# Kernel optimization log

Measured on AMD Instinct MI355X. Metric: run time of the kernel, lower is better.

Reference implementation:

```python
import jax, jax.numpy as jnp
import numpy as np

B, S, DIM = 64, 256, 512
H = 16
DH = DIM // H          # 32
W = 256                # window_size == seq_len
ROPE_BASE = 10000.0


def _rope(x):
    # x: (B, S, H, DH), interleaved-pair RoPE
    pos = jnp.arange(S, dtype=jnp.float32)
    inv_freq = 1.0 / (ROPE_BASE ** (jnp.arange(0, DH, 2, dtype=jnp.float32) / DH))
    sinusoid = pos[:, None] * inv_freq[None, :]            # (S, DH/2)
    sin = jnp.sin(sinusoid)[None, :, None, :]              # (1, S, 1, DH/2)
    cos = jnp.cos(sinusoid)[None, :, None, :]
    x1 = x[..., 0::2]
    x2 = x[..., 1::2]
    r1 = x1 * cos - x2 * sin
    r2 = x1 * sin + x2 * cos
    return jnp.stack([r1, r2], axis=-1).reshape(x.shape)


def setup_inputs() -> dict:
    key = jax.random.key(0)
    ks = jax.random.split(key, 8)
    s = 1.0 / np.sqrt(DIM)
    return {
        "hidden_states": jax.random.normal(ks[0], (B, S, DIM), jnp.float32),
        "Wq": jax.random.normal(ks[1], (DIM, DIM), jnp.float32) * s,
        "bq": jnp.zeros((DIM,), jnp.float32),
        "Wk": jax.random.normal(ks[2], (DIM, DIM), jnp.float32) * s,
        "bk": jnp.zeros((DIM,), jnp.float32),
        "Wv": jax.random.normal(ks[3], (DIM, DIM), jnp.float32) * s,
        "bv": jnp.zeros((DIM,), jnp.float32),
        "bias_table": jax.random.normal(ks[4], (2 * W - 1, H), jnp.float32) * 0.02,
    }


def reference(hidden_states, Wq, bq, Wk, bk, Wv, bv, bias_table):
    b, s, _ = hidden_states.shape
    q = hidden_states @ Wq + bq
    k = hidden_states @ Wk + bk
    v = hidden_states @ Wv + bv
    # (B, S, H, DH)
    q = _rope(q.reshape(b, s, H, DH))
    k = _rope(k.reshape(b, s, H, DH))
    v = v.reshape(b, s, H, DH)
    # (B, H, S, DH)
    q = q.transpose(0, 2, 1, 3)
    k = k.transpose(0, 2, 1, 3)
    v = v.transpose(0, 2, 1, 3)
    scores = jnp.einsum('bhqd,bhkd->bhqk', q, k) / np.sqrt(DH)
    # relative_position_index[i, j] == (i - j) + W - 1
    rel_idx = jnp.arange(W)[:, None] - jnp.arange(W)[None, :] + (W - 1)
    rel_bias = bias_table[rel_idx]                 # (W, W, H)
    rel_bias = rel_bias.transpose(2, 0, 1)[None]   # (1, H, W, W)
    # NOTE: bias added AFTER softmax, faithful to the original module
    probs = jax.nn.softmax(scores, axis=-1) + rel_bias
    ctx = jnp.einsum('bhqk,bhkd->bhqd', probs, v)
    ctx = ctx.transpose(0, 2, 1, 3).reshape(b, s, DIM)
    return ctx
```

## Files before the change

### kernel.cpp

```cpp
#include <hip/hip_runtime.h>
#include <stdint.h>

typedef __attribute__((ext_vector_type(8))) short bf16x8;
typedef __attribute__((ext_vector_type(4))) float f32x4;
typedef __attribute__((ext_vector_type(4))) unsigned int u32x4;

#define MFMA16(a, b, c) __builtin_amdgcn_mfma_f32_16x16x32_bf16(a, b, c, 0, 0, 0)

__device__ __forceinline__ float bf2f(unsigned short u) {
    union { unsigned int i; float f; } x; x.i = ((unsigned int)u) << 16; return x.f;
}
__device__ __forceinline__ unsigned short f2bf(float f) {
    union { float f; unsigned int i; } x; x.f = f;
    unsigned int u = x.i;
    return (unsigned short)((u + 0x7FFFu + ((u >> 16) & 1u)) >> 16);
}

__global__ __launch_bounds__(256) void k_cvt(const float4* __restrict__ in,
                                             unsigned short* __restrict__ out) {
    int i = blockIdx.x * 256 + threadIdx.x;
    float4 v = in[i];
    ushort4 o;
    o.x = f2bf(v.x); o.y = f2bf(v.y); o.z = f2bf(v.z); o.w = f2bf(v.w);
    *(ushort4*)(out + (size_t)i * 4) = o;
}

__global__ __launch_bounds__(256) void k_wt(const float* __restrict__ W0,
                                            const float* __restrict__ W1,
                                            const float* __restrict__ W2,
                                            unsigned short* __restrict__ Wt2) {
    int tile = blockIdx.x * 4 + (threadIdx.x >> 6);
    int l = threadIdx.x & 63;
    int nt = tile >> 4;
    int kb = tile & 15;
    int mat = nt >> 5;
    const float* __restrict__ Wm = (mat == 0) ? W0 : (mat == 1) ? W1 : W2;
    int np = (nt & 31) * 16 + (l & 15);
    int k0 = kb * 32 + (l >> 4) * 8;
    bf16x8 o;
#pragma unroll
    for (int e = 0; e < 8; ++e) o[e] = (short)f2bf(Wm[(size_t)(k0 + e) * 512 + np]);
    *(bf16x8*)(Wt2 + (size_t)tile * 512 + l * 8) = o;
}

__global__ __launch_bounds__(256) void k_sc(float* __restrict__ cs2) {
    int s = threadIdx.x;
    for (int f = 0; f < 16; ++f) {
        float inv = powf(10000.0f, -(float)f / 16.0f);
        float a = (float)s * inv;
        cs2[(s * 16 + f) * 2 + 0] = cosf(a);
        cs2[(s * 16 + f) * 2 + 1] = sinf(a);
    }
}

__global__ __launch_bounds__(256, 2) void k_gemm(
    const unsigned short* __restrict__ A,
    const unsigned short* __restrict__ Bt,
    const float* __restrict__ bq, const float* __restrict__ bk, const float* __restrict__ bv,
    const float* __restrict__ cs2,
    unsigned short* __restrict__ Qo, unsigned short* __restrict__ Ko, unsigned short* __restrict__ Vo) {
    __shared__ unsigned short a_l[2][8192];
    const int tid = threadIdx.x;
    const int wave = tid >> 6, lane = tid & 63;
    const int l15 = lane & 15, l4 = lane >> 4;
    int bid = blockIdx.x;
    int swz = (bid & 7) * 192 + (bid >> 3);
    const int m0 = (swz / 12) * 128;
    const int n0 = (swz % 12) * 128;
    const int wm = (wave >> 1) * 64, wn = (wave & 1) * 64;
    const bool isV = (n0 >= 1024);

    f32x4 zero4 = {0.f, 0.f, 0.f, 0.f};
    f32x4 acc[4][4];
#pragma unroll
    for (int i = 0; i < 4; ++i)
#pragma unroll
        for (int j = 0; j < 4; ++j) acc[i][j] = zero4;

    const int srow = tid >> 3;
    const int skc = ((tid & 7) ^ (srow & 7)) * 8;
    const unsigned short* ga = A + (size_t)(m0 + srow) * 512 + skc;
    const unsigned short* gB2 = Bt + ((size_t)((n0 + wn) >> 4) << 13) + lane * 8;

#define STAGE(buf, kt)                                                                          \
    {                                                                                           \
        const unsigned short* pa = ga + (kt) * 64;                                              \
        unsigned short* la = &a_l[(buf)][wave * 512];                                           \
        _Pragma("unroll")                                                                       \
        for (int it = 0; it < 4; ++it) {                                                        \
            __builtin_amdgcn_global_load_lds(                                                   \
                (const __attribute__((address_space(1))) unsigned int*)(pa + it * (32 * 512)),  \
                (__attribute__((address_space(3))) unsigned int*)(la + it * 2048), 16, 0, 0);   \
        }                                                                                       \
    }
#define LOADB(breg, kt)                                                                         \
    {                                                                                           \
        _Pragma("unroll")                                                                       \
        for (int kc = 0; kc < 2; ++kc)                                                          \
            _Pragma("unroll")                                                                   \
            for (int j = 0; j < 4; ++j)                                                         \
                breg[kc][j] = *(const bf16x8*)(gB2 + j * 8192 + (kt) * 1024 + kc * 512);        \
    }
#define COMPUTE(buf, breg)                                                                      \
    {                                                                                           \
        _Pragma("unroll")                                                                       \
        for (int kc = 0; kc < 2; ++kc) {                                                        \
            bf16x8 af[4];                                                                       \
            int g = ((kc * 4 + l4) ^ (l15 & 7)) * 8;                                            \
            _Pragma("unroll")                                                                   \
            for (int i = 0; i < 4; ++i)                                                         \
                af[i] = *(const bf16x8*)&a_l[(buf)][(wm + i * 16 + l15) * 64 + g];              \
            if (!isV) {                                                                         \
                _Pragma("unroll")                                                               \
                for (int i = 0; i < 4; ++i)                                                     \
                    _Pragma("unroll")                                                           \
                    for (int j = 0; j < 4; ++j)                                                 \
                        acc[i][j] = MFMA16(af[i], breg[kc][j], acc[i][j]);                      \
            } else {                                                                            \
                _Pragma("unroll")                                                               \
                for (int i = 0; i < 4; ++i)                                                     \
                    _Pragma("unroll")                                                           \
                    for (int j = 0; j < 4; ++j)                                                 \
                        acc[i][j] = MFMA16(breg[kc][j], af[i], acc[i][j]);                      \
            }                                                                                   \
        }                                                                                       \
    }
#define SYNC() { asm volatile("s_waitcnt vmcnt(0) lgkmcnt(0)" ::: "memory");                    \
                 __builtin_amdgcn_s_barrier(); }

    bf16x8 b0[2][4], b1[2][4];
    LOADB(b0, 0);
    STAGE(0, 0);
    for (int kt2 = 0; kt2 < 8; kt2 += 2) {
        SYNC();
        LOADB(b1, kt2 + 1);
        STAGE(1, kt2 + 1);
        COMPUTE(0, b0);
        SYNC();
        if (kt2 + 2 < 8) {
            LOADB(b0, kt2 + 2);
            STAGE(0, kt2 + 2);
        }
        COMPUTE(1, b1);
    }
#undef STAGE
#undef LOADB
#undef COMPUTE
#undef SYNC

    if (!isV) {
        const int mat = n0 >> 9;
        unsigned short* __restrict__ dst = (mat == 0) ? Qo : Ko;
        const float* __restrict__ bias = (mat == 0) ? bq : bk;
#pragma unroll
        for (int j = 0; j < 4; ++j) {
            int col = (n0 & 511) + wn + j * 16 + l15;
            float bb = bias[col];
            int h = col >> 5, dh = col & 31, f = dh >> 1;
            float sgn = (col & 1) ? 1.0f : -1.0f;
#pragma unroll
            for (int i = 0; i < 4; ++i) {
#pragma unroll
                for (int r = 0; r < 4; ++r) {
                    int m = m0 + wm + i * 16 + l4 * 4 + r;
                    int b2 = m >> 8, s = m & 255;
                    float t = acc[i][j][r] + bb;
                    float partner = __shfl_xor(t, 1);
                    float2 cn = *(const float2*)(cs2 + (s * 16 + f) * 2);
                    float o = t * cn.x + sgn * partner * cn.y;
                    dst[(size_t)(b2 * 16 + h) * 8192 + s * 32 + dh] = f2bf(o);
                }
            }
        }
    } else {
#pragma unroll
        for (int j = 0; j < 4; ++j) {
#pragma unroll
            for (int r = 0; r < 4; ++r) {
                int n = (n0 & 511) + wn + j * 16 + l4 * 4 + r;
                float bb = bv[n];
                int h = n >> 5, dh = n & 31;
#pragma unroll
                for (int i = 0; i < 4; ++i) {
                    int m = m0 + wm + i * 16 + l15;
                    int b2 = m >> 8, s = m & 255;
                    Vo[(size_t)(b2 * 16 + h) * 8192 + dh * 256 + s] = f2bf(acc[i][j][r] + bb);
                }
            }
        }
    }
}

__global__ __launch_bounds__(256, 2) void k_attn(
    const unsigned short* __restrict__ Qm, const unsigned short* __restrict__ Km,
    const unsigned short* __restrict__ Vm,
    const float* __restrict__ bias_table, float* __restrict__ out) {
    __shared__ unsigned short k_l[256 * 32];
    __shared__ unsigned short vt_l[32 * 256];
    __shared__ unsigned short p_l[64 * 264];
    __shared__ float bias_g[512];

    const int tid = threadIdx.x, wave = tid >> 6, lane = tid & 63;
    const int l15 = lane & 15, l4 = lane >> 4;
    int bid = blockIdx.x;
    int swz = (bid & 7) * 128 + (bid >> 3);
    const int h = swz & 15, b = swz >> 4;
    const size_t bh = ((size_t)(b * 16 + h)) * 8192;

    for (int i = tid; i < 511; i += 256) bias_g[i] = bias_table[i * 16 + h];

#pragma unroll
    for (int it = 0; it < 4; ++it) {
        int p = it * 256 + wave * 64 + lane;
        __builtin_amdgcn_global_load_lds(
            (const __attribute__((address_space(1))) unsigned int*)(Km + bh + p * 8),
            (__attribute__((address_space(3))) unsigned int*)(k_l + it * 2048 + wave * 512), 16, 0, 0);
    }
#pragma unroll
    for (int it = 0; it < 4; ++it) {
        int p = it * 256 + wave * 64 + lane;
        int dh = p >> 5, cpos = p & 31;
        int srcc = cpos ^ (dh & 7);
        __builtin_amdgcn_global_load_lds(
            (const __attribute__((address_space(1))) unsigned int*)(Vm + bh + dh * 256 + srcc * 8),
            (__attribute__((address_space(3))) unsigned int*)(vt_l + it * 2048 + wave * 512), 16, 0, 0);
    }
    __syncthreads();

    f32x4 zero4 = {0.f, 0.f, 0.f, 0.f};
    const float SCL2 = 0.17677669529663687f * 1.4426950408889634f;
    const int qrow = 16 * wave + l15;

    for (int qb = 0; qb < 4; ++qb) {
        const int q0 = qb * 64;
        bf16x8 qfrag = *(const bf16x8*)(Qm + bh + (size_t)(q0 + qrow) * 32 + l4 * 8);

        f32x4 sc[16];
#pragma unroll
        for (int ct = 0; ct < 16; ++ct) {
            bf16x8 kf = *(const bf16x8*)&k_l[(ct * 16 + l15) * 32 + l4 * 8];
            sc[ct] = MFMA16(kf, qfrag, zero4);
        }

        float sum = 0.f;
#pragma unroll
        for (int ct = 0; ct < 16; ++ct) {
#pragma unroll
            for (int r = 0; r < 4; ++r) {
                float e;
                float x = sc[ct][r] * SCL2;
                asm("v_exp_f32 %0, %1" : "=v"(e) : "v"(x));
                sc[ct][r] = e;
                sum += e;
            }
        }
        sum += __shfl_xor(sum, 16);
        sum += __shfl_xor(sum, 32);
        float inv = 1.0f / sum;

#pragma unroll
        for (int ct = 0; ct < 16; ++ct) {
            int kbase = 16 * ct + 4 * l4;
            int jb = q0 + qrow - kbase + 255;
            float p0 = sc[ct][0] * inv + bias_g[jb];
            float p1 = sc[ct][1] * inv + bias_g[jb - 1];
            float p2 = sc[ct][2] * inv + bias_g[jb - 2];
            float p3 = sc[ct][3] * inv + bias_g[jb - 3];
            uint2 w;
            w.x = (unsigned int)f2bf(p0) | ((unsigned int)f2bf(p1) << 16);
            w.y = (unsigned int)f2bf(p2) | ((unsigned int)f2bf(p3) << 16);
            *(uint2*)&p_l[qrow * 264 + kbase] = w;
        }

        f32x4 o0 = zero4, o1 = zero4;
#pragma unroll
        for (int kc = 0; kc < 8; ++kc) {
            bf16x8 pf = *(const bf16x8*)&p_l[qrow * 264 + kc * 32 + l4 * 8];
            int vc = (kc * 4 + l4) ^ (l15 & 7);
            bf16x8 v0 = *(const bf16x8*)&vt_l[l15 * 256 + vc * 8];
            bf16x8 v1 = *(const bf16x8*)&vt_l[(16 + l15) * 256 + vc * 8];
            o0 = MFMA16(pf, v0, o0);
            o1 = MFMA16(pf, v1, o1);
        }

#pragma unroll
        for (int r = 0; r < 4; ++r) {
            int s = q0 + 16 * wave + l4 * 4 + r;
            float* po = out + ((size_t)(b * 256 + s)) * 512 + h * 32;
            po[l15] = o0[r];
            po[16 + l15] = o1[r];
        }
    }
}

extern "C" void kernel_launch(void* const* d_in, const int* in_sizes, int n_in,
                              void* d_out, int out_size, void* d_ws, size_t ws_size,
                              hipStream_t stream) {
    const float* hs = (const float*)d_in[0];
    const float* Wq = (const float*)d_in[1];
    const float* bq = (const float*)d_in[2];
    const float* Wk = (const float*)d_in[3];
    const float* bk = (const float*)d_in[4];
    const float* Wv = (const float*)d_in[5];
    const float* bv = (const float*)d_in[6];
    const float* bt = (const float*)d_in[7];
    float* out = (float*)d_out;

    char* ws = (char*)d_ws;
    unsigned short* hsb = (unsigned short*)ws;
    unsigned short* wt = (unsigned short*)(ws + 16777216);
    unsigned short* Qo = (unsigned short*)(ws + 18350080);
    unsigned short* Ko = (unsigned short*)(ws + 35127296);
    unsigned short* Vo = (unsigned short*)(ws + 51904512);
    float* cs2 = (float*)(ws + 68681728);

    hipLaunchKernelGGL(k_cvt, dim3(8192), dim3(256), 0, stream, (const float4*)hs, hsb);
    hipLaunchKernelGGL(k_wt, dim3(384), dim3(256), 0, stream, Wq, Wk, Wv, wt);
    hipLaunchKernelGGL(k_sc, dim3(1), dim3(256), 0, stream, cs2);
    hipLaunchKernelGGL(k_gemm, dim3(1536), dim3(256), 0, stream,
                       hsb, wt, bq, bk, bv, cs2, Qo, Ko, Vo);
    hipLaunchKernelGGL(k_attn, dim3(1024), dim3(256), 0, stream,
                       Qo, Ko, Vo, bt, out);
}
```

Measured before the change: 100.6 us.

## Pre-tile activations for LDS-free GEMM and keep attention probs in registers

The conversion kernel now writes hidden states in an MFMA-fragment-tiled bf16 layout, so the QKV GEMM loads A and B fragments straight from global memory with no LDS staging or barriers. The GEMM tile is halved to 128x64, doubling the grid, and occupancy is raised to 3 blocks per CU. The attention kernel drops the P shared-memory buffer and rearranges the probability fragments across lanes with packed bf16 conversions and xor shuffles, allowing 4 blocks per CU. The risks are more global/L2 traffic from loads that no longer go through LDS, and extra shuffle work in the attention loop.

Measured after the change: 128.6 us. 1.28x slower.

```diff
diff --git a/kernel.cpp b/kernel.cpp
--- a/kernel.cpp
+++ b/kernel.cpp
@@ -17,12 +17,30 @@
 }
 
 __global__ __launch_bounds__(256) void k_cvt(const float4* __restrict__ in,
-                                             unsigned short* __restrict__ out) {
-    int i = blockIdx.x * 256 + threadIdx.x;
-    float4 v = in[i];
-    ushort4 o;
-    o.x = f2bf(v.x); o.y = f2bf(v.y); o.z = f2bf(v.z); o.w = f2bf(v.w);
-    *(ushort4*)(out + (size_t)i * 4) = o;
+                                             unsigned short* __restrict__ At) {
+    __shared__ unsigned short t[16 * 512];
+    const int tid = threadIdx.x;
+    const int blk = blockIdx.x;
+#pragma unroll
+    for (int it = 0; it < 8; ++it) {
+        int idx = it * 256 + tid;
+        int row = idx >> 7, col4 = idx & 127;
+        float4 v = in[(size_t)(blk * 16 + row) * 128 + col4];
+        ushort4 o;
+        o.x = f2bf(v.x); o.y = f2bf(v.y); o.z = f2bf(v.z); o.w = f2bf(v.w);
+        int addr = row * 512 + (((col4 >> 1) ^ (row & 7)) << 3) + ((col4 & 1) << 2);
+        *(ushort4*)&t[addr] = o;
+    }
+    __syncthreads();
+#pragma unroll
+    for (int it = 0; it < 4; ++it) {
+        int idx = it * 256 + tid;
+        int kb = idx >> 6, l = idx & 63;
+        int row = l & 15, l4 = l >> 4;
+        int c = (kb * 4 + l4) ^ (row & 7);
+        bf16x8 v = *(const bf16x8*)&t[row * 512 + c * 8];
+        *(bf16x8*)(At + ((size_t)(blk * 16 + kb) << 9) + l * 8) = v;
+    }
 }
 
 __global__ __launch_bounds__(256) void k_wt(const float* __restrict__ W0,
@@ -53,107 +71,58 @@
     }
 }
 
-__global__ __launch_bounds__(256, 2) void k_gemm(
-    const unsigned short* __restrict__ A,
+__global__ __launch_bounds__(256, 3) void k_gemm(
+    const unsigned short* __restrict__ At,
     const unsigned short* __restrict__ Bt,
     const float* __restrict__ bq, const float* __restrict__ bk, const float* __restrict__ bv,
     const float* __restrict__ cs2,
     unsigned short* __restrict__ Qo, unsigned short* __restrict__ Ko, unsigned short* __restrict__ Vo) {
-    __shared__ unsigned short a_l[2][8192];
     const int tid = threadIdx.x;
     const int wave = tid >> 6, lane = tid & 63;
     const int l15 = lane & 15, l4 = lane >> 4;
     int bid = blockIdx.x;
-    int swz = (bid & 7) * 192 + (bid >> 3);
-    const int m0 = (swz / 12) * 128;
-    const int n0 = (swz % 12) * 128;
-    const int wm = (wave >> 1) * 64, wn = (wave & 1) * 64;
+    int swz = (bid & 7) * 384 + (bid >> 3);
+    const int m0 = (swz / 24) * 128;
+    const int n0 = (swz % 24) * 64;
+    const int wm = (wave >> 1) * 64, wn = (wave & 1) * 32;
     const bool isV = (n0 >= 1024);
 
     f32x4 zero4 = {0.f, 0.f, 0.f, 0.f};
-    f32x4 acc[4][4];
+    f32x4 acc[4][2];
 #pragma unroll
     for (int i = 0; i < 4; ++i)
 #pragma unroll
-        for (int j = 0; j < 4; ++j) acc[i][j] = zero4;
-
-    const int srow = tid >> 3;
-    const int skc = ((tid & 7) ^ (srow & 7)) * 8;
-    const unsigned short* ga = A + (size_t)(m0 + srow) * 512 + skc;
-    const unsigned short* gB2 = Bt + ((size_t)((n0 + wn) >> 4) << 13) + lane * 8;
-
-#define STAGE(buf, kt)                                                                          \
-    {                                                                                           \
-        const unsigned short* pa = ga + (kt) * 64;                                              \
-        unsigned short* la = &a_l[(buf)][wave * 512];                                           \
-        _Pragma("unroll")                                                                       \
-        for (int it = 0; it < 4; ++it) {                                                        \
-            __builtin_amdgcn_global_load_lds(                                                   \
-                (const __attribute__((address_space(1))) unsigned int*)(pa + it * (32 * 512)),  \
-                (__attribute__((address_space(3))) unsigned int*)(la + it * 2048), 16, 0, 0);   \
-        }                                                                                       \
-    }
-#define LOADB(breg, kt)                                                                         \
-    {                                                                                           \
-        _Pragma("unroll")                                                                       \
-        for (int kc = 0; kc < 2; ++kc)                                                          \
-            _Pragma("unroll")                                                                   \
-            for (int j = 0; j < 4; ++j)                                                         \
-                breg[kc][j] = *(const bf16x8*)(gB2 + j * 8192 + (kt) * 1024 + kc * 512);        \
-    }
-#define COMPUTE(buf, breg)                                                                      \
-    {                                                                                           \
-        _Pragma("unroll")                                                                       \
-        for (int kc = 0; kc < 2; ++kc) {                                                        \
-            bf16x8 af[4];                                                                       \
-            int g = ((kc * 4 + l4) ^ (l15 & 7)) * 8;                                            \
-            _Pragma("unroll")                                                                   \
-            for (int i = 0; i < 4; ++i)                                                         \
-                af[i] = *(const bf16x8*)&a_l[(buf)][(wm + i * 16 + l15) * 64 + g];              \
-            if (!isV) {                                                                         \
-                _Pragma("unroll")                                                               \
-                for (int i = 0; i < 4; ++i)                                                     \
-                    _Pragma("unroll")                                                           \
-                    for (int j = 0; j < 4; ++j)                                                 \
-                        acc[i][j] = MFMA16(af[i], breg[kc][j], acc[i][j]);                      \
-            } else {                                                                            \
-                _Pragma("unroll")                                                               \
-                for (int i = 0; i < 4; ++i)                                                     \
-                    _Pragma("unroll")                                                           \
-                    for (int j = 0; j < 4; ++j)                                                 \
-                        acc[i][j] = MFMA16(breg[kc][j], af[i], acc[i][j]);                      \
-            }                                                                                   \
-        }                                                                                       \
-    }
-#define SYNC() { asm volatile("s_waitcnt vmcnt(0) lgkmcnt(0)" ::: "memory");                    \
-                 __builtin_amdgcn_s_barrier(); }
-
-    bf16x8 b0[2][4], b1[2][4];
-    LOADB(b0, 0);
-    STAGE(0, 0);
-    for (int kt2 = 0; kt2 < 8; kt2 += 2) {
-        SYNC();
-        LOADB(b1, kt2 + 1);
-        STAGE(1, kt2 + 1);
-        COMPUTE(0, b0);
-        SYNC();
-        if (kt2 + 2 < 8) {
-            LOADB(b0, kt2 + 2);
-            STAGE(0, kt2 + 2);
-        }
-        COMPUTE(1, b1);
-    }
-#undef STAGE
-#undef LOADB
-#undef COMPUTE
-#undef SYNC
+        for (int j = 0; j < 2; ++j) acc[i][j] = zero4;
+
+    const unsigned short* gA = At + ((size_t)((m0 + wm) >> 4) << 13) + lane * 8;
+    const unsigned short* gB = Bt + ((size_t)((n0 + wn) >> 4) << 13) + lane * 8;
+
+#pragma unroll
+    for (int kb = 0; kb < 16; ++kb) {
+        bf16x8 af[4], bf[2];
+#pragma unroll
+        for (int i = 0; i < 4; ++i) af[i] = *(const bf16x8*)(gA + (size_t)i * 8192 + kb * 512);
+#pragma unroll
+        for (int j = 0; j < 2; ++j) bf[j] = *(const bf16x8*)(gB + (size_t)j * 8192 + kb * 512);
+        if (!isV) {
+#pragma unroll
+            for (int i = 0; i < 4; ++i)
+#pragma unroll
+                for (int j = 0; j < 2; ++j) acc[i][j] = MFMA16(af[i], bf[j], acc[i][j]);
+        } else {
+#pragma unroll
+            for (int i = 0; i < 4; ++i)
+#pragma unroll
+                for (int j = 0; j < 2; ++j) acc[i][j] = MFMA16(bf[j], af[i], acc[i][j]);
+        }
+    }
 
     if (!isV) {
         const int mat = n0 >> 9;
         unsigned short* __restrict__ dst = (mat == 0) ? Qo : Ko;
         const float* __restrict__ bias = (mat == 0) ? bq : bk;
 #pragma unroll
-        for (int j = 0; j < 4; ++j) {
+        for (int j = 0; j < 2; ++j) {
             int col = (n0 & 511) + wn + j * 16 + l15;
             float bb = bias[col];
             int h = col >> 5, dh = col & 31, f = dh >> 1;
@@ -174,7 +143,7 @@
         }
     } else {
 #pragma unroll
-        for (int j = 0; j < 4; ++j) {
+        for (int j = 0; j < 2; ++j) {
 #pragma unroll
             for (int r = 0; r < 4; ++r) {
                 int n = (n0 & 511) + wn + j * 16 + l4 * 4 + r;
@@ -191,13 +160,12 @@
     }
 }
 
-__global__ __launch_bounds__(256, 2) void k_attn(
+__global__ __launch_bounds__(256, 4) void k_attn(
     const unsigned short* __restrict__ Qm, const unsigned short* __restrict__ Km,
     const unsigned short* __restrict__ Vm,
     const float* __restrict__ bias_table, float* __restrict__ out) {
     __shared__ unsigned short k_l[256 * 32];
     __shared__ unsigned short vt_l[32 * 256];
-    __shared__ unsigned short p_l[64 * 264];
     __shared__ float bias_g[512];
 
     const int tid = threadIdx.x, wave = tid >> 6, lane = tid & 63;
@@ -230,6 +198,8 @@
     f32x4 zero4 = {0.f, 0.f, 0.f, 0.f};
     const float SCL2 = 0.17677669529663687f * 1.4426950408889634f;
     const int qrow = 16 * wave + l15;
+    const bool hi = (l4 >> 1) != 0;
+    const bool odd = (l4 & 1) != 0;
 
     for (int qb = 0; qb < 4; ++qb) {
         const int q0 = qb * 64;
@@ -258,29 +228,43 @@
         sum += __shfl_xor(sum, 32);
         float inv = 1.0f / sum;
 
-#pragma unroll
-        for (int ct = 0; ct < 16; ++ct) {
-            int kbase = 16 * ct + 4 * l4;
-            int jb = q0 + qrow - kbase + 255;
-            float p0 = sc[ct][0] * inv + bias_g[jb];
-            float p1 = sc[ct][1] * inv + bias_g[jb - 1];
-            float p2 = sc[ct][2] * inv + bias_g[jb - 2];
-            float p3 = sc[ct][3] * inv + bias_g[jb - 3];
-            uint2 w;
-            w.x = (unsigned int)f2bf(p0) | ((unsigned int)f2bf(p1) << 16);
-            w.y = (unsigned int)f2bf(p2) | ((unsigned int)f2bf(p3) << 16);
-            *(uint2*)&p_l[qrow * 264 + kbase] = w;
-        }
-
         f32x4 o0 = zero4, o1 = zero4;
 #pragma unroll
-        for (int kc = 0; kc < 8; ++kc) {
-            bf16x8 pf = *(const bf16x8*)&p_l[qrow * 264 + kc * 32 + l4 * 8];
-            int vc = (kc * 4 + l4) ^ (l15 & 7);
+        for (int m = 0; m < 8; ++m) {
+            unsigned int E0, E1, O0, O1;
+            {
+                int kbase = 32 * m + 4 * l4;
+                int jb = q0 + qrow - kbase + 255;
+                float p0 = sc[2 * m][0] * inv + bias_g[jb];
+                float p1 = sc[2 * m][1] * inv + bias_g[jb - 1];
+                float p2 = sc[2 * m][2] * inv + bias_g[jb - 2];
+                float p3 = sc[2 * m][3] * inv + bias_g[jb - 3];
+                asm("v_cvt_pk_bf16_f32 %0, %1, %2" : "=v"(E0) : "v"(p0), "v"(p1));
+                asm("v_cvt_pk_bf16_f32 %0, %1, %2" : "=v"(E1) : "v"(p2), "v"(p3));
+                jb -= 16;
+                p0 = sc[2 * m + 1][0] * inv + bias_g[jb];
+                p1 = sc[2 * m + 1][1] * inv + bias_g[jb - 1];
+                p2 = sc[2 * m + 1][2] * inv + bias_g[jb - 2];
+                p3 = sc[2 * m + 1][3] * inv + bias_g[jb - 3];
+                asm("v_cvt_pk_bf16_f32 %0, %1, %2" : "=v"(O0) : "v"(p0), "v"(p1));
+                asm("v_cvt_pk_bf16_f32 %0, %1, %2" : "=v"(O1) : "v"(p2), "v"(p3));
+            }
+            unsigned int m0_ = hi ? O0 : E0, m1_ = hi ? O1 : E1;
+            unsigned int s0 = hi ? E0 : O0, s1 = hi ? E1 : O1;
+            unsigned int g0 = __shfl_xor(s0, 32), g1 = __shfl_xor(s1, 32);
+            unsigned int X00 = hi ? g0 : m0_, X01 = hi ? g1 : m1_;
+            unsigned int X10 = hi ? m0_ : g0, X11 = hi ? m1_ : g1;
+            unsigned int k0 = odd ? X10 : X00, k1 = odd ? X11 : X01;
+            unsigned int t0 = odd ? X00 : X10, t1 = odd ? X01 : X11;
+            unsigned int r0 = __shfl_xor(t0, 16), r1 = __shfl_xor(t1, 16);
+            union { unsigned int u[4]; bf16x8 v; } pu;
+            pu.u[0] = odd ? r0 : k0; pu.u[1] = odd ? r1 : k1;
+            pu.u[2] = odd ? k0 : r0; pu.u[3] = odd ? k1 : r1;
+            int vc = (m * 4 + l4) ^ (l15 & 7);
             bf16x8 v0 = *(const bf16x8*)&vt_l[l15 * 256 + vc * 8];
             bf16x8 v1 = *(const bf16x8*)&vt_l[(16 + l15) * 256 + vc * 8];
-            o0 = MFMA16(pf, v0, o0);
-            o1 = MFMA16(pf, v1, o1);
+            o0 = MFMA16(pu.v, v0, o0);
+            o1 = MFMA16(pu.v, v1, o1);
         }
 
 #pragma unroll
@@ -314,10 +298,10 @@
     unsigned short* Vo = (unsigned short*)(ws + 51904512);
     float* cs2 = (float*)(ws + 68681728);
 
-    hipLaunchKernelGGL(k_cvt, dim3(8192), dim3(256), 0, stream, (const float4*)hs, hsb);
+    hipLaunchKernelGGL(k_cvt, dim3(1024), dim3(256), 0, stream, (const float4*)hs, hsb);
     hipLaunchKernelGGL(k_wt, dim3(384), dim3(256), 0, stream, Wq, Wk, Wv, wt);
     hipLaunchKernelGGL(k_sc, dim3(1), dim3(256), 0, stream, cs2);
-    hipLaunchKernelGGL(k_gemm, dim3(1536), dim3(256), 0, stream,
+    hipLaunchKernelGGL(k_gemm, dim3(3072), dim3(256), 0, stream,
                        hsb, wt, bq, bk, bv, cs2, Qo, Ko, Vo);
     hipLaunchKernelGGL(k_attn, dim3(1024), dim3(256), 0, stream,
                        Qo, Ko, Vo, bt, out);
```
